# Performance work log

Measured on AMD Instinct MI355X. Metric: run time of the kernel, lower is better.

The kernel has to match this reference:

```python
import jax, jax.numpy as jnp
import numpy as np

NUM_REGIONS = 4
REGION_OVERLAP = 0.25
REGIONAL_WEIGHT = 0.6


def setup_inputs() -> dict:
    key = jax.random.key(0)
    features = jax.random.normal(key, (8, 128, 128, 512), dtype=jnp.float32)
    return {"features": features}


def reference(features):
    # features: (B, H, W, D)
    N = NUM_REGIONS
    rw = REGIONAL_WEIGHT
    B, H, W, D = features.shape

    # Global mean over spatial dims (keepdim, broadcasts over H, W)
    global_feat = features.mean(axis=(1, 2), keepdims=True)  # (B,1,1,D)

    # Overlapping region extraction + per-region mean pooling
    region_h, region_w = H // N, W // N
    oh, ow = int(region_h * REGION_OVERLAP), int(region_w * REGION_OVERLAP)
    sh, sw = region_h - oh, region_w - ow
    means = []
    for i in range(N):            # fixed small grid (4x4 = 16 regions)
        for j in range(N):
            h0, w0 = i * sh, j * sw
            h1, w1 = min(h0 + region_h, H), min(w0 + region_w, W)
            means.append(features[:, h0:h1, w0:w1, :].mean(axis=(1, 2)))
    means = jnp.stack(means, axis=1)  # (B, N*N, D), region index r = i*N + j

    # Gaussian weights: exp(-d^2 / (2*0.5^2)) = exp(-2*d^2), d = |coord - i| / N
    h_coords = jnp.linspace(0.0, N - 1, H)  # (H,)
    w_coords = jnp.linspace(0.0, N - 1, W)  # (W,)
    idx = jnp.arange(N, dtype=jnp.float32)
    hw = jnp.exp(-2.0 * ((h_coords[None, :] - idx[:, None]) / N) ** 2)  # (N,H)
    ww = jnp.exp(-2.0 * ((w_coords[None, :] - idx[:, None]) / N) ** 2)  # (N,W)
    Wmat = (hw[:, None, :, None] * ww[None, :, None, :]).reshape(N * N, H, W)

    wsum = Wmat.sum(axis=0)[None, :, :, None]  # (1,H,W,1)
    # Weighted broadcast-aggregate of region means back to pixels
    agg = jnp.einsum('rhw,brd->bhwd', Wmat, means) / (wsum + 1e-8)

    enhanced = (1.0 - rw) * global_feat + rw * agg + features
    return enhanced
```

## Files before the change

kernel.cpp:

```cpp
#include <hip/hip_runtime.h>
#include <math.h>

#define BB 8
#define HH 128
#define WW 128
#define DD 512

typedef __attribute__((ext_vector_type(4))) float fvec4;

__device__ __forceinline__ float4 f4z() { return make_float4(0.f, 0.f, 0.f, 0.f); }
__device__ __forceinline__ float4 f4add(float4 a, float4 b) {
    return make_float4(a.x + b.x, a.y + b.y, a.z + b.z, a.w + b.w);
}
__device__ __forceinline__ float4 f4fma(float s, float4 a, float4 acc) {
    return make_float4(fmaf(s, a.x, acc.x), fmaf(s, a.y, acc.y),
                       fmaf(s, a.z, acc.z), fmaf(s, a.w, acc.w));
}
__device__ __forceinline__ float4 f4scale(float4 a, float s) {
    return make_float4(a.x * s, a.y * s, a.z * s, a.w * s);
}

__global__ __launch_bounds__(512) void k1_rowsums(const float* __restrict__ f,
                                                  float* __restrict__ rowpart,
                                                  float* __restrict__ rowtot) {
    const int bh = blockIdx.x;
    const int tid = threadIdx.x;
    const int dt = tid & 127;
    const int g = tid >> 7;
    const int d4 = dt * 4;

    const float4* p = (const float4*)(f + (size_t)bh * WW * DD) + (size_t)g * (DD / 4) + dt;

    float4 tot = f4z(), r0 = f4z(), r1 = f4z(), r2 = f4z(), r3 = f4z();

#define SEG(I0, I1, STMT)                                  \
    _Pragma("unroll")                                      \
    for (int it = (I0); it < (I1); ++it) {                 \
        float4 v = p[(size_t)it * 4 * (DD / 4)];           \
        tot = f4add(tot, v);                               \
        STMT                                               \
    }
    SEG(0, 6,   r0 = f4add(r0, v);)
    SEG(6, 8,   r0 = f4add(r0, v); r1 = f4add(r1, v);)
    SEG(8, 12,  r1 = f4add(r1, v);)
    SEG(12, 14, r1 = f4add(r1, v); r2 = f4add(r2, v);)
    SEG(14, 18, r2 = f4add(r2, v);)
    SEG(18, 20, r2 = f4add(r2, v); r3 = f4add(r3, v);)
    SEG(20, 26, r3 = f4add(r3, v);)
    SEG(26, 32, )
#undef SEG

    __shared__ float4 lds[3][5][128];
    if (g > 0) {
        lds[g - 1][0][dt] = r0;
        lds[g - 1][1][dt] = r1;
        lds[g - 1][2][dt] = r2;
        lds[g - 1][3][dt] = r3;
        lds[g - 1][4][dt] = tot;
    }
    __syncthreads();
    if (g == 0) {
#pragma unroll
        for (int gg = 0; gg < 3; ++gg) {
            r0 = f4add(r0, lds[gg][0][dt]);
            r1 = f4add(r1, lds[gg][1][dt]);
            r2 = f4add(r2, lds[gg][2][dt]);
            r3 = f4add(r3, lds[gg][3][dt]);
            tot = f4add(tot, lds[gg][4][dt]);
        }
        float4* rp = (float4*)(rowpart + ((size_t)bh * 4) * DD + d4);
        rp[0 * (DD / 4)] = r0;
        rp[1 * (DD / 4)] = r1;
        rp[2 * (DD / 4)] = r2;
        rp[3 * (DD / 4)] = r3;
        *(float4*)(rowtot + (size_t)bh * DD + d4) = tot;
    }
}

__global__ __launch_bounds__(128) void k2_reduce(const float* __restrict__ rowpart,
                                                 const float* __restrict__ rowtot,
                                                 float* __restrict__ means,
                                                 float* __restrict__ gmean) {
    const int blk = blockIdx.x;
    const int d4 = threadIdx.x * 4;
    if (blk < BB * 16) {
        const int b = blk >> 4;
        const int r = blk & 15;
        const int i = r >> 2;
        const int j = r & 3;
        const int h0 = i * 24;
        float4 s = f4z();
#pragma unroll 8
        for (int hh = 0; hh < 32; ++hh) {
            const int bh = b * HH + h0 + hh;
            s = f4add(s, *(const float4*)(rowpart + ((size_t)bh * 4 + j) * DD + d4));
        }
        s = f4scale(s, 1.0f / 1024.0f);
        *(float4*)(means + ((size_t)b * 16 + r) * DD + d4) = s;
    } else {
        const int b = blk - BB * 16;
        float4 s = f4z();
#pragma unroll 8
        for (int h = 0; h < HH; ++h) {
            s = f4add(s, *(const float4*)(rowtot + (size_t)(b * HH + h) * DD + d4));
        }
        s = f4scale(s, 1.0f / (float)(HH * WW));
        *(float4*)(gmean + (size_t)b * DD + d4) = s;
    }
}

__global__ __launch_bounds__(512) void k3_output(const float* __restrict__ f,
                                                 const float* __restrict__ means,
                                                 const float* __restrict__ gmean,
                                                 float* __restrict__ out) {
    const int bh = blockIdx.x;
    const int b = bh / HH;
    const int h = bh % HH;
    const int tid = threadIdx.x;
    const int dt = tid & 127;
    const int g = tid >> 7;
    const int d4 = dt * 4;

    __shared__ float4 sww[WW];

    const float hc = (3.0f / 127.0f) * (float)h;
    float hwv[4];
    float Hs = 0.f;
#pragma unroll
    for (int i = 0; i < 4; ++i) {
        const float t = (hc - (float)i) * 0.25f;
        hwv[i] = __expf(-2.0f * t * t);
        Hs += hwv[i];
    }

    if (tid < WW) {
        const float wc = (3.0f / 127.0f) * (float)tid;
        float wv[4];
        float Ws = 0.f;
#pragma unroll
        for (int j = 0; j < 4; ++j) {
            const float t = (wc - (float)j) * 0.25f;
            wv[j] = __expf(-2.0f * t * t);
            Ws += wv[j];
        }
        const float inv = 0.6f / (Hs * Ws + 1e-8f);
        sww[tid] = make_float4(wv[0] * inv, wv[1] * inv, wv[2] * inv, wv[3] * inv);
    }
    __syncthreads();

    float4 cs0 = f4z(), cs1 = f4z(), cs2 = f4z(), cs3 = f4z();
#pragma unroll
    for (int i = 0; i < 4; ++i) {
        const float hwi = hwv[i];
        const float4* mrow = (const float4*)(means + ((size_t)b * 16 + i * 4) * DD + d4);
        cs0 = f4fma(hwi, mrow[0 * (DD / 4)], cs0);
        cs1 = f4fma(hwi, mrow[1 * (DD / 4)], cs1);
        cs2 = f4fma(hwi, mrow[2 * (DD / 4)], cs2);
        cs3 = f4fma(hwi, mrow[3 * (DD / 4)], cs3);
    }
    const float4 gv = *(const float4*)(gmean + (size_t)b * DD + d4);
    const float4 gterm = f4scale(gv, 0.4f);

    const float4* fp = (const float4*)(f + (size_t)bh * WW * DD) + (size_t)g * (DD / 4) + dt;
    float* op = out + (size_t)bh * WW * DD + (size_t)g * DD + d4;

#pragma unroll 8
    for (int it = 0; it < 32; ++it) {
        const int w = it * 4 + g;
        const float4 v = fp[(size_t)it * 4 * (DD / 4)];
        const float4 wwv = sww[w];
        fvec4 o;
        o.x = v.x + gterm.x + (cs0.x * wwv.x + cs1.x * wwv.y + cs2.x * wwv.z + cs3.x * wwv.w);
        o.y = v.y + gterm.y + (cs0.y * wwv.x + cs1.y * wwv.y + cs2.y * wwv.z + cs3.y * wwv.w);
        o.z = v.z + gterm.z + (cs0.z * wwv.x + cs1.z * wwv.y + cs2.z * wwv.z + cs3.z * wwv.w);
        o.w = v.w + gterm.w + (cs0.w * wwv.x + cs1.w * wwv.y + cs2.w * wwv.z + cs3.w * wwv.w);
        __builtin_nontemporal_store(o, (fvec4*)(op + (size_t)it * 4 * DD));
    }
}

extern "C" void kernel_launch(void* const* d_in, const int* in_sizes, int n_in,
                              void* d_out, int out_size, void* d_ws, size_t ws_size,
                              hipStream_t stream) {
    const float* f = (const float*)d_in[0];
    float* out = (float*)d_out;

    float* ws = (float*)d_ws;
    float* rowpart = ws;
    float* rowtot = rowpart + (size_t)BB * HH * 4 * DD;
    float* means = rowtot + (size_t)BB * HH * DD;
    float* gmean = means + (size_t)BB * 16 * DD;

    k1_rowsums<<<BB * HH, 512, 0, stream>>>(f, rowpart, rowtot);
    k2_reduce<<<BB * 16 + BB, 128, 0, stream>>>(rowpart, rowtot, means, gmean);
    k3_output<<<BB * HH, 512, 0, stream>>>(f, means, gmean, out);
}
```

Baseline: 497.8 us.

## Fuse three passes into one cooperative kernel processing batches in two halves

Replaces the three-kernel sequence with a single cooperative persistent kernel of 512 blocks that handles half the batch at a time, separated by grid-wide syncs. The intent is that each half's slice of features (64 MB) may still be resident in cache when the output pass rereads it, cutting DRAM traffic and removing launch gaps. It also spreads the second-stage reduction across more threads and switches the feature reads in the output pass to nontemporal loads. The costs are four grid.sync barriers and a requirement that all 512 blocks be co-resident, with a fallback to the old three-kernel path if the cooperative launch fails.

```diff
diff --git a/kernel.cpp b/kernel.cpp
--- a/kernel.cpp
+++ b/kernel.cpp
@@ -1,10 +1,17 @@
 #include <hip/hip_runtime.h>
+#include <hip/hip_cooperative_groups.h>
 #include <math.h>
+
+namespace cg = cooperative_groups;
 
 #define BB 8
 #define HH 128
 #define WW 128
 #define DD 512
+#define GB 4
+#define NG 2
+#define GRID (GB * HH)
+#define THR 512
 
 typedef __attribute__((ext_vector_type(4))) float fvec4;
 
@@ -20,11 +27,10 @@
     return make_float4(a.x * s, a.y * s, a.z * s, a.w * s);
 }
 
-__global__ __launch_bounds__(512) void k1_rowsums(const float* __restrict__ f,
-                                                  float* __restrict__ rowpart,
-                                                  float* __restrict__ rowtot) {
-    const int bh = blockIdx.x;
-    const int tid = threadIdx.x;
+__device__ __forceinline__ void p1_row(const float* __restrict__ f,
+                                       float* __restrict__ rowpart,
+                                       float* __restrict__ rowtot,
+                                       int bh, int tid, float4 lds1[3][5][128]) {
     const int dt = tid & 127;
     const int g = tid >> 7;
     const int d4 = dt * 4;
@@ -50,23 +56,22 @@
     SEG(26, 32, )
 #undef SEG
 
-    __shared__ float4 lds[3][5][128];
     if (g > 0) {
-        lds[g - 1][0][dt] = r0;
-        lds[g - 1][1][dt] = r1;
-        lds[g - 1][2][dt] = r2;
-        lds[g - 1][3][dt] = r3;
-        lds[g - 1][4][dt] = tot;
+        lds1[g - 1][0][dt] = r0;
+        lds1[g - 1][1][dt] = r1;
+        lds1[g - 1][2][dt] = r2;
+        lds1[g - 1][3][dt] = r3;
+        lds1[g - 1][4][dt] = tot;
     }
     __syncthreads();
     if (g == 0) {
 #pragma unroll
         for (int gg = 0; gg < 3; ++gg) {
-            r0 = f4add(r0, lds[gg][0][dt]);
-            r1 = f4add(r1, lds[gg][1][dt]);
-            r2 = f4add(r2, lds[gg][2][dt]);
-            r3 = f4add(r3, lds[gg][3][dt]);
-            tot = f4add(tot, lds[gg][4][dt]);
+            r0 = f4add(r0, lds1[gg][0][dt]);
+            r1 = f4add(r1, lds1[gg][1][dt]);
+            r2 = f4add(r2, lds1[gg][2][dt]);
+            r3 = f4add(r3, lds1[gg][3][dt]);
+            tot = f4add(tot, lds1[gg][4][dt]);
         }
         float4* rp = (float4*)(rowpart + ((size_t)bh * 4) * DD + d4);
         rp[0 * (DD / 4)] = r0;
@@ -75,6 +80,150 @@
         rp[3 * (DD / 4)] = r3;
         *(float4*)(rowtot + (size_t)bh * DD + d4) = tot;
     }
+}
+
+__device__ __forceinline__ void p2(const float* __restrict__ rowpart,
+                                   const float* __restrict__ rowtot,
+                                   float* __restrict__ means,
+                                   float* __restrict__ gmean,
+                                   int b0, int blk, int tid, float4 l2buf[3][128]) {
+    if (blk >= GB * 17) return;
+    const int bl = blk / 17;
+    const int o = blk % 17;
+    const int b = b0 + bl;
+    const int dt = tid & 127;
+    const int q = tid >> 7;
+    const int d4 = dt * 4;
+
+    float4 s = f4z();
+    if (o < 16) {
+        const int i = o >> 2;
+        const int j = o & 3;
+        const int h0 = i * 24;
+#pragma unroll
+        for (int hh = 0; hh < 8; ++hh) {
+            const int bh = b * HH + h0 + q * 8 + hh;
+            s = f4add(s, *(const float4*)(rowpart + ((size_t)bh * 4 + j) * DD + d4));
+        }
+    } else {
+#pragma unroll 8
+        for (int hh = 0; hh < 32; ++hh) {
+            const int bh = b * HH + q * 32 + hh;
+            s = f4add(s, *(const float4*)(rowtot + (size_t)bh * DD + d4));
+        }
+    }
+    if (q > 0) l2buf[q - 1][dt] = s;
+    __syncthreads();
+    if (q == 0) {
+#pragma unroll
+        for (int qq = 0; qq < 3; ++qq) s = f4add(s, l2buf[qq][dt]);
+        if (o < 16)
+            *(float4*)(means + ((size_t)b * 16 + o) * DD + d4) = f4scale(s, 1.0f / 1024.0f);
+        else
+            *(float4*)(gmean + (size_t)b * DD + d4) = f4scale(s, 1.0f / (float)(HH * WW));
+    }
+}
+
+__device__ __forceinline__ void p3_row(const float* __restrict__ f,
+                                       const float* __restrict__ means,
+                                       const float* __restrict__ gmean,
+                                       float* __restrict__ out,
+                                       int bh, int b, int tid,
+                                       const float4* sww, const float* hwv) {
+    const int dt = tid & 127;
+    const int g = tid >> 7;
+    const int d4 = dt * 4;
+
+    float4 cs0 = f4z(), cs1 = f4z(), cs2 = f4z(), cs3 = f4z();
+#pragma unroll
+    for (int i = 0; i < 4; ++i) {
+        const float hwi = hwv[i];
+        const float4* mrow = (const float4*)(means + ((size_t)b * 16 + i * 4) * DD + d4);
+        cs0 = f4fma(hwi, mrow[0 * (DD / 4)], cs0);
+        cs1 = f4fma(hwi, mrow[1 * (DD / 4)], cs1);
+        cs2 = f4fma(hwi, mrow[2 * (DD / 4)], cs2);
+        cs3 = f4fma(hwi, mrow[3 * (DD / 4)], cs3);
+    }
+    const float4 gv = *(const float4*)(gmean + (size_t)b * DD + d4);
+    const float4 gterm = f4scale(gv, 0.4f);
+
+    const float* fp = f + (size_t)bh * WW * DD + (size_t)g * DD + d4;
+    float* op = out + (size_t)bh * WW * DD + (size_t)g * DD + d4;
+
+#pragma unroll 8
+    for (int it = 0; it < 32; ++it) {
+        const int w = it * 4 + g;
+        const fvec4 v = __builtin_nontemporal_load((const fvec4*)(fp + (size_t)it * 4 * DD));
+        const float4 wwv = sww[w];
+        fvec4 o;
+        o.x = v.x + gterm.x + (cs0.x * wwv.x + cs1.x * wwv.y + cs2.x * wwv.z + cs3.x * wwv.w);
+        o.y = v.y + gterm.y + (cs0.y * wwv.x + cs1.y * wwv.y + cs2.y * wwv.z + cs3.y * wwv.w);
+        o.z = v.z + gterm.z + (cs0.z * wwv.x + cs1.z * wwv.y + cs2.z * wwv.z + cs3.z * wwv.w);
+        o.w = v.w + gterm.w + (cs0.w * wwv.x + cs1.w * wwv.y + cs2.w * wwv.z + cs3.w * wwv.w);
+        __builtin_nontemporal_store(o, (fvec4*)(op + (size_t)it * 4 * DD));
+    }
+}
+
+__global__ __launch_bounds__(THR, 4) void fused_all(const float* __restrict__ f,
+                                                    float* __restrict__ rowpart,
+                                                    float* __restrict__ rowtot,
+                                                    float* __restrict__ means,
+                                                    float* __restrict__ gmean,
+                                                    float* __restrict__ out) {
+    __shared__ float4 lds1[3][5][128];
+    __shared__ float4 l2buf[3][128];
+    __shared__ float4 sww[WW];
+
+    cg::grid_group grid = cg::this_grid();
+    const int blk = blockIdx.x;
+    const int tid = threadIdx.x;
+    const int bl = blk >> 7;
+    const int h = blk & 127;
+
+    const float hc = (3.0f / 127.0f) * (float)h;
+    float hwv[4];
+    float Hs = 0.f;
+#pragma unroll
+    for (int i = 0; i < 4; ++i) {
+        const float t = (hc - (float)i) * 0.25f;
+        hwv[i] = __expf(-2.0f * t * t);
+        Hs += hwv[i];
+    }
+    if (tid < WW) {
+        const float wc = (3.0f / 127.0f) * (float)tid;
+        float wv[4];
+        float Ws = 0.f;
+#pragma unroll
+        for (int j = 0; j < 4; ++j) {
+            const float t = (wc - (float)j) * 0.25f;
+            wv[j] = __expf(-2.0f * t * t);
+            Ws += wv[j];
+        }
+        const float inv = 0.6f / (Hs * Ws + 1e-8f);
+        sww[tid] = make_float4(wv[0] * inv, wv[1] * inv, wv[2] * inv, wv[3] * inv);
+    }
+    __syncthreads();
+
+    const int b_g0 = 0 * GB + bl;
+    const int b_g1 = 1 * GB + bl;
+
+    p1_row(f, rowpart, rowtot, b_g0 * HH + h, tid, lds1);
+    grid.sync();
+    p2(rowpart, rowtot, means, gmean, 0 * GB, blk, tid, l2buf);
+    grid.sync();
+    p3_row(f, means, gmean, out, b_g0 * HH + h, b_g0, tid, sww, hwv);
+    p1_row(f, rowpart, rowtot, b_g1 * HH + h, tid, lds1);
+    grid.sync();
+    p2(rowpart, rowtot, means, gmean, 1 * GB, blk, tid, l2buf);
+    grid.sync();
+    p3_row(f, means, gmean, out, b_g1 * HH + h, b_g1, tid, sww, hwv);
+}
+
+__global__ __launch_bounds__(512) void k1_rowsums(const float* __restrict__ f,
+                                                  float* __restrict__ rowpart,
+                                                  float* __restrict__ rowtot) {
+    __shared__ float4 lds1[3][5][128];
+    p1_row(f, rowpart, rowtot, blockIdx.x, threadIdx.x, lds1);
 }
 
 __global__ __launch_bounds__(128) void k2_reduce(const float* __restrict__ rowpart,
@@ -95,8 +244,7 @@
             const int bh = b * HH + h0 + hh;
             s = f4add(s, *(const float4*)(rowpart + ((size_t)bh * 4 + j) * DD + d4));
         }
-        s = f4scale(s, 1.0f / 1024.0f);
-        *(float4*)(means + ((size_t)b * 16 + r) * DD + d4) = s;
+        *(float4*)(means + ((size_t)b * 16 + r) * DD + d4) = f4scale(s, 1.0f / 1024.0f);
     } else {
         const int b = blk - BB * 16;
         float4 s = f4z();
@@ -104,8 +252,7 @@
         for (int h = 0; h < HH; ++h) {
             s = f4add(s, *(const float4*)(rowtot + (size_t)(b * HH + h) * DD + d4));
         }
-        s = f4scale(s, 1.0f / (float)(HH * WW));
-        *(float4*)(gmean + (size_t)b * DD + d4) = s;
+        *(float4*)(gmean + (size_t)b * DD + d4) = f4scale(s, 1.0f / (float)(HH * WW));
     }
 }
 
@@ -113,15 +260,11 @@
                                                  const float* __restrict__ means,
                                                  const float* __restrict__ gmean,
                                                  float* __restrict__ out) {
+    __shared__ float4 sww[WW];
     const int bh = blockIdx.x;
     const int b = bh / HH;
     const int h = bh % HH;
     const int tid = threadIdx.x;
-    const int dt = tid & 127;
-    const int g = tid >> 7;
-    const int d4 = dt * 4;
-
-    __shared__ float4 sww[WW];
 
     const float hc = (3.0f / 127.0f) * (float)h;
     float hwv[4];
@@ -132,7 +275,6 @@
         hwv[i] = __expf(-2.0f * t * t);
         Hs += hwv[i];
     }
-
     if (tid < WW) {
         const float wc = (3.0f / 127.0f) * (float)tid;
         float wv[4];
@@ -147,35 +289,7 @@
         sww[tid] = make_float4(wv[0] * inv, wv[1] * inv, wv[2] * inv, wv[3] * inv);
     }
     __syncthreads();
-
-    float4 cs0 = f4z(), cs1 = f4z(), cs2 = f4z(), cs3 = f4z();
-#pragma unroll
-    for (int i = 0; i < 4; ++i) {
-        const float hwi = hwv[i];
-        const float4* mrow = (const float4*)(means + ((size_t)b * 16 + i * 4) * DD + d4);
-        cs0 = f4fma(hwi, mrow[0 * (DD / 4)], cs0);
-        cs1 = f4fma(hwi, mrow[1 * (DD / 4)], cs1);
-        cs2 = f4fma(hwi, mrow[2 * (DD / 4)], cs2);
-        cs3 = f4fma(hwi, mrow[3 * (DD / 4)], cs3);
-    }
-    const float4 gv = *(const float4*)(gmean + (size_t)b * DD + d4);
-    const float4 gterm = f4scale(gv, 0.4f);
-
-    const float4* fp = (const float4*)(f + (size_t)bh * WW * DD) + (size_t)g * (DD / 4) + dt;
-    float* op = out + (size_t)bh * WW * DD + (size_t)g * DD + d4;
-
-#pragma unroll 8
-    for (int it = 0; it < 32; ++it) {
-        const int w = it * 4 + g;
-        const float4 v = fp[(size_t)it * 4 * (DD / 4)];
-        const float4 wwv = sww[w];
-        fvec4 o;
-        o.x = v.x + gterm.x + (cs0.x * wwv.x + cs1.x * wwv.y + cs2.x * wwv.z + cs3.x * wwv.w);
-        o.y = v.y + gterm.y + (cs0.y * wwv.x + cs1.y * wwv.y + cs2.y * wwv.z + cs3.y * wwv.w);
-        o.z = v.z + gterm.z + (cs0.z * wwv.x + cs1.z * wwv.y + cs2.z * wwv.z + cs3.z * wwv.w);
-        o.w = v.w + gterm.w + (cs0.w * wwv.x + cs1.w * wwv.y + cs2.w * wwv.z + cs3.w * wwv.w);
-        __builtin_nontemporal_store(o, (fvec4*)(op + (size_t)it * 4 * DD));
-    }
+    p3_row(f, means, gmean, out, bh, b, tid, sww, hwv);
 }
 
 extern "C" void kernel_launch(void* const* d_in, const int* in_sizes, int n_in,
@@ -190,7 +304,13 @@
     float* means = rowtot + (size_t)BB * HH * DD;
     float* gmean = means + (size_t)BB * 16 * DD;
 
-    k1_rowsums<<<BB * HH, 512, 0, stream>>>(f, rowpart, rowtot);
-    k2_reduce<<<BB * 16 + BB, 128, 0, stream>>>(rowpart, rowtot, means, gmean);
-    k3_output<<<BB * HH, 512, 0, stream>>>(f, means, gmean, out);
-}
+    void* args[] = {(void*)&f, (void*)&rowpart, (void*)&rowtot,
+                    (void*)&means, (void*)&gmean, (void*)&out};
+    hipError_t e = hipLaunchCooperativeKernel((const void*)fused_all, dim3(GRID),
+                                              dim3(THR), args, 0, stream);
+    if (e != hipSuccess) {
+        k1_rowsums<<<BB * HH, 512, 0, stream>>>(f, rowpart, rowtot);
+        k2_reduce<<<BB * 16 + BB, 128, 0, stream>>>(rowpart, rowtot, means, gmean);
+        k3_output<<<BB * HH, 512, 0, stream>>>(f, means, gmean, out);
+    }
+}
```

Measured after the change: 702.6 us. +41.2%, slower.
